# Kernel tuning notes

Measured on AMD Instinct MI355X. Metric: run time of the kernel, lower is better.

Reference implementation:

```python
import jax, jax.numpy as jnp
import numpy as np

EMBED_DIM = 1024
NUM_HEADS = 16
HEAD_DIM = EMBED_DIM // NUM_HEADS


def setup_inputs() -> dict:
    key = jax.random.key(0)
    k1, k2, k3, k4, k5 = jax.random.split(key, 5)
    C = EMBED_DIM
    x = jax.random.normal(k1, (4, 2048, C), dtype=jnp.float32)
    s = 1.0 / np.sqrt(C)
    qkv_w = jax.random.uniform(k2, (3 * C, C), jnp.float32, -s, s)
    qkv_b = jax.random.uniform(k3, (3 * C,), jnp.float32, -s, s)
    proj_w = jax.random.uniform(k4, (C, C), jnp.float32, -s, s)
    proj_b = jax.random.uniform(k5, (C,), jnp.float32, -s, s)
    return {"x": x, "qkv_w": qkv_w, "qkv_b": qkv_b, "proj_w": proj_w, "proj_b": proj_b}


def reference(x, qkv_w, qkv_b, proj_w, proj_b):
    B, T, C = x.shape
    H, D = NUM_HEADS, HEAD_DIM
    qkv = jnp.einsum('btc,oc->bto', x, qkv_w) + qkv_b  # [B,T,3C]
    q, k, v = jnp.split(qkv, 3, axis=2)
    # [B,T,C] -> [B,H,T,D]
    q = q.reshape(B, T, H, D).transpose(0, 2, 1, 3)
    k = k.reshape(B, T, H, D).transpose(0, 2, 1, 3)
    v = v.reshape(B, T, H, D).transpose(0, 2, 1, 3)
    scores = jnp.einsum('bhqd,bhkd->bhqk', q, k) / jnp.sqrt(jnp.float32(D)).astype(q.dtype)
    causal = jnp.tril(jnp.ones((T, T), dtype=bool))
    scores = jnp.where(causal[None, None], scores, jnp.finfo(scores.dtype).min)
    attn = jax.nn.softmax(scores, axis=-1)
    out = jnp.einsum('bhqk,bhkd->bhqd', attn, v)
    out = out.transpose(0, 2, 1, 3).reshape(B, T, C)
    return jnp.einsum('btc,oc->bto', out, proj_w) + proj_b
```

## Files before the change

kernel.cpp:

```cpp
#include <hip/hip_runtime.h>

#define EMBED 1024
#define C3    3072
#define NHEAD 16
#define HDIM  64
#define BB    4
#define TT    2048
#define MTOK  8192

typedef __bf16 bf16;
typedef __bf16 bf16x4 __attribute__((ext_vector_type(4)));
typedef __bf16 bf16x8 __attribute__((ext_vector_type(8)));
typedef float  f32x4  __attribute__((ext_vector_type(4)));
typedef float  f32x16 __attribute__((ext_vector_type(16)));
typedef unsigned int u32;

__device__ __forceinline__ void gload_lds16(const bf16* g, bf16* l) {
  __builtin_amdgcn_global_load_lds((__attribute__((address_space(1))) void*)g,
                                   (__attribute__((address_space(3))) void*)l,
                                   16, 0, 0);
}

__device__ __forceinline__ u32 pkbf(float lo, float hi_) {
  union { bf16 h[2]; u32 w; } u;
  u.h[0] = (bf16)lo; u.h[1] = (bf16)hi_;
  return u.w;
}

__global__ __launch_bounds__(256) void cvt_kernel(const float* __restrict__ in,
                                                  bf16* __restrict__ out, int n) {
  int i = (blockIdx.x * blockDim.x + threadIdx.x) * 4;
  if (i >= n) return;
  float4 v = *reinterpret_cast<const float4*>(in + i);
  bf16x4 o;
  o[0] = (bf16)v.x; o[1] = (bf16)v.y; o[2] = (bf16)v.z; o[3] = (bf16)v.w;
  *reinterpret_cast<bf16x4*>(out + i) = o;
}

__global__ __launch_bounds__(256) void gemm_qkv(const bf16* __restrict__ A,
                                                const bf16* __restrict__ W,
                                                const float* __restrict__ bias,
                                                bf16* __restrict__ Qh,
                                                bf16* __restrict__ Kh,
                                                bf16* __restrict__ VhT) {
  const int K = EMBED;
  __shared__ __align__(16) bf16 lA[128 * 32];
  __shared__ __align__(16) bf16 lB[128 * 32];
  const int tid  = threadIdx.x;
  const int lane = tid & 63;
  const int wave = tid >> 6;
  const int wm   = (wave >> 1) * 64;
  const int wn   = (wave & 1) * 64;
  const int bn0  = blockIdx.x * 128;
  const int bm0  = blockIdx.y * 128;
  const int l15  = lane & 15, lg = lane >> 4;
  const int srow = tid >> 2;
  const int sseg = tid & 3;

  f32x4 acc[4][4] = {};

  for (int kt = 0; kt < K; kt += 32) {
#pragma unroll
    for (int c = 0; c < 2; ++c) {
      int row = c * 64 + srow;
      gload_lds16(A + (size_t)(bm0 + row) * K + kt + sseg * 8, &lA[(c * 256 + tid) * 8]);
      gload_lds16(W + (size_t)(bn0 + row) * K + kt + sseg * 8, &lB[(c * 256 + tid) * 8]);
    }
    __syncthreads();
    bf16x8 af[4], bf_[4];
#pragma unroll
    for (int i = 0; i < 4; ++i)
      af[i] = *reinterpret_cast<const bf16x8*>(&lA[(wm + i * 16 + l15) * 32 + lg * 8]);
#pragma unroll
    for (int j = 0; j < 4; ++j)
      bf_[j] = *reinterpret_cast<const bf16x8*>(&lB[(wn + j * 16 + l15) * 32 + lg * 8]);
#pragma unroll
    for (int i = 0; i < 4; ++i)
#pragma unroll
      for (int j = 0; j < 4; ++j)
        acc[i][j] = __builtin_amdgcn_mfma_f32_16x16x32_bf16(af[i], bf_[j], acc[i][j], 0, 0, 0);
    __syncthreads();
  }

  const int sec = bn0 >> 10;
#pragma unroll
  for (int i = 0; i < 4; ++i)
#pragma unroll
    for (int j = 0; j < 4; ++j) {
      const int col = bn0 + wn + j * 16 + l15;
      const float bs = bias[col];
      const int c2 = col & 1023, hh = c2 >> 6, dd = c2 & 63;
      const int rowb = bm0 + wm + i * 16 + lg * 4;
      const int bb = rowb >> 11, t0 = rowb & 2047;
      const int bh = bb * 16 + hh;
      if (sec < 2) {
        bf16* dst = (sec ? Kh : Qh) + ((size_t)bh * TT + t0) * HDIM + dd;
#pragma unroll
        for (int r = 0; r < 4; ++r) dst[(size_t)r * HDIM] = (bf16)(acc[i][j][r] + bs);
      } else {
        bf16x4 o4;
#pragma unroll
        for (int r = 0; r < 4; ++r) o4[r] = (bf16)(acc[i][j][r] + bs);
        *reinterpret_cast<bf16x4*>(VhT + ((size_t)bh * HDIM + dd) * TT + t0) = o4;
      }
    }
}

__global__ __launch_bounds__(256) void gemm_bt(const bf16* __restrict__ A,
                                               const bf16* __restrict__ W,
                                               const float* __restrict__ bias,
                                               float* __restrict__ Cf,
                                               int M, int N, int K) {
  __shared__ __align__(16) bf16 lA[128 * 32];
  __shared__ __align__(16) bf16 lB[128 * 32];
  const int tid  = threadIdx.x;
  const int lane = tid & 63;
  const int wave = tid >> 6;
  const int wm   = (wave >> 1) * 64;
  const int wn   = (wave & 1) * 64;
  const int bn0  = blockIdx.x * 128;
  const int bm0  = blockIdx.y * 128;
  const int l15  = lane & 15, lg = lane >> 4;
  const int srow = tid >> 2;
  const int sseg = tid & 3;

  f32x4 acc[4][4] = {};

  for (int kt = 0; kt < K; kt += 32) {
#pragma unroll
    for (int c = 0; c < 2; ++c) {
      int row = c * 64 + srow;
      gload_lds16(A + (size_t)(bm0 + row) * K + kt + sseg * 8, &lA[(c * 256 + tid) * 8]);
      gload_lds16(W + (size_t)(bn0 + row) * K + kt + sseg * 8, &lB[(c * 256 + tid) * 8]);
    }
    __syncthreads();
    bf16x8 af[4], bf_[4];
#pragma unroll
    for (int i = 0; i < 4; ++i)
      af[i] = *reinterpret_cast<const bf16x8*>(&lA[(wm + i * 16 + l15) * 32 + lg * 8]);
#pragma unroll
    for (int j = 0; j < 4; ++j)
      bf_[j] = *reinterpret_cast<const bf16x8*>(&lB[(wn + j * 16 + l15) * 32 + lg * 8]);
#pragma unroll
    for (int i = 0; i < 4; ++i)
#pragma unroll
      for (int j = 0; j < 4; ++j)
        acc[i][j] = __builtin_amdgcn_mfma_f32_16x16x32_bf16(af[i], bf_[j], acc[i][j], 0, 0, 0);
    __syncthreads();
  }

#pragma unroll
  for (int i = 0; i < 4; ++i)
#pragma unroll
    for (int j = 0; j < 4; ++j) {
      int col = bn0 + wn + j * 16 + l15;
      float bs = bias[col];
#pragma unroll
      for (int r = 0; r < 4; ++r) {
        int row = bm0 + wm + i * 16 + lg * 4 + r;
        Cf[(size_t)row * N + col] = acc[i][j][r] + bs;
      }
    }
}

__device__ __forceinline__ void attn_tile(const char* kbase, const char* vbase,
                                          const bf16x8 (&qfr)[4], f32x16 (&oacc)[2],
                                          float& mrun, float& srun,
                                          const int kv0, const int q0w,
                                          const int l31, const int hi, const int swz) {
  f32x16 s0 = {}, s1 = {};
  __builtin_amdgcn_s_setprio(1);
#pragma unroll
  for (int dc = 0; dc < 4; ++dc) {
    bf16x8 kf = *reinterpret_cast<const bf16x8*>(
        kbase + l31 * 128 + (((2 * dc + hi) * 16) ^ swz));
    s0 = __builtin_amdgcn_mfma_f32_32x32x16_bf16(kf, qfr[dc], s0, 0, 0, 0);
  }
#pragma unroll
  for (int dc = 0; dc < 4; ++dc) {
    bf16x8 kf = *reinterpret_cast<const bf16x8*>(
        kbase + (32 + l31) * 128 + (((2 * dc + hi) * 16) ^ swz));
    s1 = __builtin_amdgcn_mfma_f32_32x32x16_bf16(kf, qfr[dc], s1, 0, 0, 0);
  }
  __builtin_amdgcn_s_setprio(0);

  if (kv0 + 63 > q0w) {
    const int qg = q0w + l31;
#pragma unroll
    for (int r = 0; r < 16; ++r) {
      const int kvb = kv0 + (r & 3) + 8 * (r >> 2) + 4 * hi;
      if (kvb > qg)      s0[r] = -3e38f;
      if (kvb + 32 > qg) s1[r] = -3e38f;
    }
  }

  float m8[8];
#pragma unroll
  for (int i = 0; i < 8; ++i)
    m8[i] = fmaxf(fmaxf(s0[i], s0[i + 8]), fmaxf(s1[i], s1[i + 8]));
#pragma unroll
  for (int st = 4; st > 0; st >>= 1)
#pragma unroll
    for (int i = 0; i < st; ++i) m8[i] = fmaxf(m8[i], m8[i + st]);
  float mx = fmaxf(m8[0], __shfl_xor(m8[0], 32));

  float mref = mrun;
  if (!__all(mx <= mrun + 8.0f)) {
    const float mnew = fmaxf(mrun, mx);
    const float corr = __builtin_amdgcn_exp2f(mrun - mnew);
    mrun = mnew; mref = mnew;
    srun *= corr;
#pragma unroll
    for (int r = 0; r < 16; ++r) { oacc[0][r] *= corr; oacc[1][r] *= corr; }
  }

  float psum = 0.0f;
#pragma unroll
  for (int r = 0; r < 16; ++r) {
    s0[r] = __builtin_amdgcn_exp2f(s0[r] - mref);
    s1[r] = __builtin_amdgcn_exp2f(s1[r] - mref);
    psum += s0[r] + s1[r];
  }
  srun += psum;

  union { u32 w[4]; bf16x8 v; } pw[4];
#pragma unroll
  for (int cl = 0; cl < 2; ++cl) {
    {
      u32 a01 = pkbf(s0[8 * cl + 0], s0[8 * cl + 1]);
      u32 a23 = pkbf(s0[8 * cl + 2], s0[8 * cl + 3]);
      u32 b01 = pkbf(s0[8 * cl + 4], s0[8 * cl + 5]);
      u32 b23 = pkbf(s0[8 * cl + 6], s0[8 * cl + 7]);
      asm("v_permlane32_swap_b32 %0, %1" : "+v"(a01), "+v"(b01));
      asm("v_permlane32_swap_b32 %0, %1" : "+v"(a23), "+v"(b23));
      pw[cl].w[0] = a01; pw[cl].w[1] = a23; pw[cl].w[2] = b01; pw[cl].w[3] = b23;
    }
    {
      u32 a01 = pkbf(s1[8 * cl + 0], s1[8 * cl + 1]);
      u32 a23 = pkbf(s1[8 * cl + 2], s1[8 * cl + 3]);
      u32 b01 = pkbf(s1[8 * cl + 4], s1[8 * cl + 5]);
      u32 b23 = pkbf(s1[8 * cl + 6], s1[8 * cl + 7]);
      asm("v_permlane32_swap_b32 %0, %1" : "+v"(a01), "+v"(b01));
      asm("v_permlane32_swap_b32 %0, %1" : "+v"(a23), "+v"(b23));
      pw[2 + cl].w[0] = a01; pw[2 + cl].w[1] = a23; pw[2 + cl].w[2] = b01; pw[2 + cl].w[3] = b23;
    }
  }

  __builtin_amdgcn_s_setprio(1);
#pragma unroll
  for (int dh = 0; dh < 2; ++dh) {
    const char* vrow = vbase + (32 * dh + l31) * 128;
#pragma unroll
    for (int c = 0; c < 4; ++c) {
      bf16x8 vf = *reinterpret_cast<const bf16x8*>(vrow + (((2 * c + hi) * 16) ^ swz));
      oacc[dh] = __builtin_amdgcn_mfma_f32_32x32x16_bf16(vf, pw[c].v, oacc[dh], 0, 0, 0);
    }
  }
  __builtin_amdgcn_s_setprio(0);
}

__global__ __launch_bounds__(256, 2) void attn_kernel(const bf16* __restrict__ Qh,
                                                      const bf16* __restrict__ Kh,
                                                      const bf16* __restrict__ VhT,
                                                      bf16* __restrict__ aout) {
  __shared__ __align__(16) bf16 lK[2][64 * 64];
  __shared__ __align__(16) bf16 lVT[2][64 * 64];
  const int tid  = threadIdx.x;
  const int lane = tid & 63, wave = tid >> 6;
  const int l31  = lane & 31;
  const int hi   = lane >> 5;
  const int bid  = blockIdx.x;
  const int bh   = bid & 63;
  const int p    = bid >> 6;
  const int qtH  = 15 - p, qtL = p;
  const int b    = bh >> 4, h = bh & 15;
  const int q0H  = qtH * 128 + wave * 32;
  const int q0L  = qtL * 128 + wave * 32;
  const size_t tb = (size_t)b * TT;
  const int swz  = (l31 & 7) << 4;

  const float QSCALE = 0.18033688011112042f;
  bf16x8 qfrH[4], qfrL[4];
  {
    const bf16* qrowH = Qh + ((size_t)bh * TT + q0H + l31) * HDIM;
    const bf16* qrowL = Qh + ((size_t)bh * TT + q0L + l31) * HDIM;
#pragma unroll
    for (int dc = 0; dc < 4; ++dc) {
      bf16x8 vH = *reinterpret_cast<const bf16x8*>(qrowH + dc * 16 + hi * 8);
      bf16x8 vL = *reinterpret_cast<const bf16x8*>(qrowL + dc * 16 + hi * 8);
      bf16x8 oH, oL;
#pragma unroll
      for (int j = 0; j < 8; ++j) {
        oH[j] = (bf16)((float)vH[j] * QSCALE);
        oL[j] = (bf16)((float)vL[j] * QSCALE);
      }
      qfrH[dc] = oH; qfrL[dc] = oL;
    }
  }

  f32x16 oaccH[2] = {}, oaccL[2] = {};
  float mH = -3e38f, sH = 0.0f, mL = -3e38f, sL = 0.0f;

  const int r0 = tid >> 3, sg = tid & 7;
  const bf16* kS0 = Kh + ((size_t)bh * TT + r0) * HDIM + (size_t)(sg ^ (r0 & 7)) * 8;
  const bf16* kS1 = Kh + ((size_t)bh * TT + 32 + r0) * HDIM + (size_t)(sg ^ (r0 & 7)) * 8;
  const bf16* vS0 = VhT + ((size_t)bh * HDIM + r0) * TT + (size_t)(sg ^ (r0 & 7)) * 8;
  const bf16* vS1 = VhT + ((size_t)bh * HDIM + 32 + r0) * TT + (size_t)(sg ^ (r0 & 7)) * 8;

  const int nkv = 2 * qtH + 2;

  gload_lds16(kS0, &lK[0][tid * 8]);
  gload_lds16(kS1, &lK[0][(tid + 256) * 8]);
  gload_lds16(vS0, &lVT[0][tid * 8]);
  gload_lds16(vS1, &lVT[0][(tid + 256) * 8]);
  __syncthreads();

  int cur = 0;
  for (int t = 0; t < nkv; ++t) {
    const int kv0 = t * 64;
    if (t + 1 < nkv) {
      const int kvn = kv0 + 64;
      gload_lds16(kS0 + (size_t)kvn * HDIM, &lK[cur ^ 1][tid * 8]);
      gload_lds16(kS1 + (size_t)kvn * HDIM, &lK[cur ^ 1][(tid + 256) * 8]);
      gload_lds16(vS0 + kvn, &lVT[cur ^ 1][tid * 8]);
      gload_lds16(vS1 + kvn, &lVT[cur ^ 1][(tid + 256) * 8]);
    }

    const char* kbase = (const char*)&lK[cur][0];
    const char* vbase = (const char*)&lVT[cur][0];
    if (kv0 <= q0H + 31)
      attn_tile(kbase, vbase, qfrH, oaccH, mH, sH, kv0, q0H, l31, hi, swz);
    if (kv0 <= q0L + 31)
      attn_tile(kbase, vbase, qfrL, oaccL, mL, sL, kv0, q0L, l31, hi, swz);

    __syncthreads();
    cur ^= 1;
  }

#pragma unroll
  for (int band = 0; band < 2; ++band) {
    const f32x16* oacc = band ? oaccL : oaccH;
    float sr = band ? sL : sH;
    sr += __shfl_xor(sr, 32);
    const float inv = 1.0f / sr;
    const int q = (band ? q0L : q0H) + l31;
    bf16* orow = aout + (tb + q) * (size_t)EMBED + h * HDIM;
#pragma unroll
    for (int dh = 0; dh < 2; ++dh)
#pragma unroll
      for (int rb = 0; rb < 4; ++rb) {
        bf16x4 o4;
#pragma unroll
        for (int k = 0; k < 4; ++k) o4[k] = (bf16)(oacc[dh][4 * rb + k] * inv);
        *reinterpret_cast<bf16x4*>(orow + 32 * dh + 8 * rb + 4 * hi) = o4;
      }
  }
}

extern "C" void kernel_launch(void* const* d_in, const int* in_sizes, int n_in,
                              void* d_out, int out_size, void* d_ws, size_t ws_size,
                              hipStream_t stream) {
  const float* x      = (const float*)d_in[0];
  const float* qkv_w  = (const float*)d_in[1];
  const float* qkv_b  = (const float*)d_in[2];
  const float* proj_w = (const float*)d_in[3];
  const float* proj_b = (const float*)d_in[4];
  float* out = (float*)d_out;

  const size_t QSZ = (size_t)BB * NHEAD * TT * HDIM;
  char* ws = (char*)d_ws;
  bf16* xb    = (bf16*)ws;
  bf16* wqkv  = xb + (size_t)MTOK * EMBED;
  bf16* wproj = wqkv + (size_t)C3 * EMBED;
  bf16* Qh    = wproj + (size_t)EMBED * EMBED;
  bf16* Kh    = Qh + QSZ;
  bf16* VhT   = Kh + QSZ;
  bf16* aob   = xb;

  cvt_kernel<<<dim3((MTOK * EMBED / 4 + 255) / 256), dim3(256), 0, stream>>>(x, xb, MTOK * EMBED);
  cvt_kernel<<<dim3((C3 * EMBED / 4 + 255) / 256), dim3(256), 0, stream>>>(qkv_w, wqkv, C3 * EMBED);
  cvt_kernel<<<dim3((EMBED * EMBED / 4 + 255) / 256), dim3(256), 0, stream>>>(proj_w, wproj, EMBED * EMBED);

  gemm_qkv<<<dim3(C3 / 128, MTOK / 128), dim3(256), 0, stream>>>(xb, wqkv, qkv_b, Qh, Kh, VhT);

  attn_kernel<<<dim3(512), dim3(256), 0, stream>>>(Qh, Kh, VhT, aob);

  gemm_bt<<<dim3(EMBED / 128, MTOK / 128), dim3(256), 0, stream>>>(
      aob, wproj, proj_b, out, MTOK, EMBED, EMBED);
}
```

Measured before the change: 177.4 us.

## Drop LDS staging in attention, per-wave KV loop; widen GEMM K-tile with swizzle

```diff
diff --git a/kernel.cpp b/kernel.cpp
--- a/kernel.cpp
+++ b/kernel.cpp
@@ -26,6 +26,8 @@
   u.h[0] = (bf16)lo; u.h[1] = (bf16)hi_;
   return u.w;
 }
+
+union upw { u32 w[4]; bf16x8 v; };
 
 __global__ __launch_bounds__(256) void cvt_kernel(const float* __restrict__ in,
                                                   bf16* __restrict__ out, int n) {
@@ -37,50 +39,70 @@
   *reinterpret_cast<bf16x4*>(out + i) = o;
 }
 
+__device__ __forceinline__ void gemm_core(const bf16* __restrict__ A,
+                                          const bf16* __restrict__ W,
+                                          int K, int bm0, int bn0,
+                                          int wm, int wn, int l15, int lg,
+                                          f32x4 (&acc)[4][4]) {
+  __shared__ __align__(16) bf16 lA[128 * 64];
+  __shared__ __align__(16) bf16 lB[128 * 64];
+  const int tid  = threadIdx.x;
+  const int grow = tid >> 3;
+  const int gseg = tid & 7;
+
+  for (int kt = 0; kt < K; kt += 64) {
+#pragma unroll
+    for (int r = 0; r < 4; ++r) {
+      const int row = r * 32 + grow;
+      const int seg = gseg ^ (row & 7);
+      gload_lds16(A + (size_t)(bm0 + row) * K + kt + seg * 8, &lA[(r * 256 + tid) * 8]);
+      gload_lds16(W + (size_t)(bn0 + row) * K + kt + seg * 8, &lB[(r * 256 + tid) * 8]);
+    }
+    __syncthreads();
+    const char* Ab = (const char*)lA;
+    const char* Bb = (const char*)lB;
+#pragma unroll
+    for (int kk = 0; kk < 2; ++kk) {
+      bf16x8 af[4], bf_[4];
+#pragma unroll
+      for (int i = 0; i < 4; ++i) {
+        const int row = wm + i * 16 + l15;
+        af[i] = *reinterpret_cast<const bf16x8*>(
+            Ab + row * 128 + ((kk * 64 + lg * 16) ^ ((row & 7) << 4)));
+      }
+#pragma unroll
+      for (int j = 0; j < 4; ++j) {
+        const int row = wn + j * 16 + l15;
+        bf_[j] = *reinterpret_cast<const bf16x8*>(
+            Bb + row * 128 + ((kk * 64 + lg * 16) ^ ((row & 7) << 4)));
+      }
+#pragma unroll
+      for (int i = 0; i < 4; ++i)
+#pragma unroll
+        for (int j = 0; j < 4; ++j)
+          acc[i][j] = __builtin_amdgcn_mfma_f32_16x16x32_bf16(af[i], bf_[j],
+                                                              acc[i][j], 0, 0, 0);
+    }
+    __syncthreads();
+  }
+}
+
 __global__ __launch_bounds__(256) void gemm_qkv(const bf16* __restrict__ A,
                                                 const bf16* __restrict__ W,
                                                 const float* __restrict__ bias,
                                                 bf16* __restrict__ Qh,
                                                 bf16* __restrict__ Kh,
                                                 bf16* __restrict__ VhT) {
-  const int K = EMBED;
-  __shared__ __align__(16) bf16 lA[128 * 32];
-  __shared__ __align__(16) bf16 lB[128 * 32];
   const int tid  = threadIdx.x;
-  const int lane = tid & 63;
-  const int wave = tid >> 6;
+  const int lane = tid & 63, wave = tid >> 6;
   const int wm   = (wave >> 1) * 64;
   const int wn   = (wave & 1) * 64;
   const int bn0  = blockIdx.x * 128;
   const int bm0  = blockIdx.y * 128;
   const int l15  = lane & 15, lg = lane >> 4;
-  const int srow = tid >> 2;
-  const int sseg = tid & 3;
 
   f32x4 acc[4][4] = {};
-
-  for (int kt = 0; kt < K; kt += 32) {
-#pragma unroll
-    for (int c = 0; c < 2; ++c) {
-      int row = c * 64 + srow;
-      gload_lds16(A + (size_t)(bm0 + row) * K + kt + sseg * 8, &lA[(c * 256 + tid) * 8]);
-      gload_lds16(W + (size_t)(bn0 + row) * K + kt + sseg * 8, &lB[(c * 256 + tid) * 8]);
-    }
-    __syncthreads();
-    bf16x8 af[4], bf_[4];
-#pragma unroll
-    for (int i = 0; i < 4; ++i)
-      af[i] = *reinterpret_cast<const bf16x8*>(&lA[(wm + i * 16 + l15) * 32 + lg * 8]);
-#pragma unroll
-    for (int j = 0; j < 4; ++j)
-      bf_[j] = *reinterpret_cast<const bf16x8*>(&lB[(wn + j * 16 + l15) * 32 + lg * 8]);
-#pragma unroll
-    for (int i = 0; i < 4; ++i)
-#pragma unroll
-      for (int j = 0; j < 4; ++j)
-        acc[i][j] = __builtin_amdgcn_mfma_f32_16x16x32_bf16(af[i], bf_[j], acc[i][j], 0, 0, 0);
-    __syncthreads();
-  }
+  gemm_core(A, W, EMBED, bm0, bn0, wm, wn, l15, lg, acc);
 
   const int sec = bn0 >> 10;
 #pragma unroll
@@ -111,43 +133,16 @@
                                                const float* __restrict__ bias,
                                                float* __restrict__ Cf,
                                                int M, int N, int K) {
-  __shared__ __align__(16) bf16 lA[128 * 32];
-  __shared__ __align__(16) bf16 lB[128 * 32];
   const int tid  = threadIdx.x;
-  const int lane = tid & 63;
-  const int wave = tid >> 6;
+  const int lane = tid & 63, wave = tid >> 6;
   const int wm   = (wave >> 1) * 64;
   const int wn   = (wave & 1) * 64;
   const int bn0  = blockIdx.x * 128;
   const int bm0  = blockIdx.y * 128;
   const int l15  = lane & 15, lg = lane >> 4;
-  const int srow = tid >> 2;
-  const int sseg = tid & 3;
 
   f32x4 acc[4][4] = {};
-
-  for (int kt = 0; kt < K; kt += 32) {
-#pragma unroll
-    for (int c = 0; c < 2; ++c) {
-      int row = c * 64 + srow;
-      gload_lds16(A + (size_t)(bm0 + row) * K + kt + sseg * 8, &lA[(c * 256 + tid) * 8]);
-      gload_lds16(W + (size_t)(bn0 + row) * K + kt + sseg * 8, &lB[(c * 256 + tid) * 8]);
-    }
-    __syncthreads();
-    bf16x8 af[4], bf_[4];
-#pragma unroll
-    for (int i = 0; i < 4; ++i)
-      af[i] = *reinterpret_cast<const bf16x8*>(&lA[(wm + i * 16 + l15) * 32 + lg * 8]);
-#pragma unroll
-    for (int j = 0; j < 4; ++j)
-      bf_[j] = *reinterpret_cast<const bf16x8*>(&lB[(wn + j * 16 + l15) * 32 + lg * 8]);
-#pragma unroll
-    for (int i = 0; i < 4; ++i)
-#pragma unroll
-      for (int j = 0; j < 4; ++j)
-        acc[i][j] = __builtin_amdgcn_mfma_f32_16x16x32_bf16(af[i], bf_[j], acc[i][j], 0, 0, 0);
-    __syncthreads();
-  }
+  gemm_core(A, W, K, bm0, bn0, wm, wn, l15, lg, acc);
 
 #pragma unroll
   for (int i = 0; i < 4; ++i)
@@ -163,47 +158,26 @@
     }
 }
 
-__device__ __forceinline__ void attn_tile(const char* kbase, const char* vbase,
-                                          const bf16x8 (&qfr)[4], f32x16 (&oacc)[2],
-                                          float& mrun, float& srun,
-                                          const int kv0, const int q0w,
-                                          const int l31, const int hi, const int swz) {
-  f32x16 s0 = {}, s1 = {};
-  __builtin_amdgcn_s_setprio(1);
-#pragma unroll
-  for (int dc = 0; dc < 4; ++dc) {
-    bf16x8 kf = *reinterpret_cast<const bf16x8*>(
-        kbase + l31 * 128 + (((2 * dc + hi) * 16) ^ swz));
-    s0 = __builtin_amdgcn_mfma_f32_32x32x16_bf16(kf, qfr[dc], s0, 0, 0, 0);
-  }
-#pragma unroll
-  for (int dc = 0; dc < 4; ++dc) {
-    bf16x8 kf = *reinterpret_cast<const bf16x8*>(
-        kbase + (32 + l31) * 128 + (((2 * dc + hi) * 16) ^ swz));
-    s1 = __builtin_amdgcn_mfma_f32_32x32x16_bf16(kf, qfr[dc], s1, 0, 0, 0);
-  }
-  __builtin_amdgcn_s_setprio(0);
-
-  if (kv0 + 63 > q0w) {
+__device__ __forceinline__ void sm_pack(f32x16& s, float& mrun, float& srun,
+                                        f32x16 (&oacc)[2], upw (&pw)[2],
+                                        const int kv0, const int q0w,
+                                        const int l31, const int hi) {
+  if (kv0 + 31 > q0w) {
     const int qg = q0w + l31;
 #pragma unroll
     for (int r = 0; r < 16; ++r) {
       const int kvb = kv0 + (r & 3) + 8 * (r >> 2) + 4 * hi;
-      if (kvb > qg)      s0[r] = -3e38f;
-      if (kvb + 32 > qg) s1[r] = -3e38f;
-    }
-  }
-
+      if (kvb > qg) s[r] = -3e38f;
+    }
+  }
   float m8[8];
 #pragma unroll
-  for (int i = 0; i < 8; ++i)
-    m8[i] = fmaxf(fmaxf(s0[i], s0[i + 8]), fmaxf(s1[i], s1[i + 8]));
+  for (int i = 0; i < 8; ++i) m8[i] = fmaxf(s[i], s[i + 8]);
 #pragma unroll
   for (int st = 4; st > 0; st >>= 1)
 #pragma unroll
     for (int i = 0; i < st; ++i) m8[i] = fmaxf(m8[i], m8[i + st]);
-  float mx = fmaxf(m8[0], __shfl_xor(m8[0], 32));
-
+  const float mx = fmaxf(m8[0], __shfl_xor(m8[0], 32));
   float mref = mrun;
   if (!__all(mx <= mrun + 8.0f)) {
     const float mnew = fmaxf(mrun, mx);
@@ -213,58 +187,29 @@
 #pragma unroll
     for (int r = 0; r < 16; ++r) { oacc[0][r] *= corr; oacc[1][r] *= corr; }
   }
-
   float psum = 0.0f;
 #pragma unroll
   for (int r = 0; r < 16; ++r) {
-    s0[r] = __builtin_amdgcn_exp2f(s0[r] - mref);
-    s1[r] = __builtin_amdgcn_exp2f(s1[r] - mref);
-    psum += s0[r] + s1[r];
+    s[r] = __builtin_amdgcn_exp2f(s[r] - mref);
+    psum += s[r];
   }
   srun += psum;
-
-  union { u32 w[4]; bf16x8 v; } pw[4];
 #pragma unroll
   for (int cl = 0; cl < 2; ++cl) {
-    {
-      u32 a01 = pkbf(s0[8 * cl + 0], s0[8 * cl + 1]);
-      u32 a23 = pkbf(s0[8 * cl + 2], s0[8 * cl + 3]);
-      u32 b01 = pkbf(s0[8 * cl + 4], s0[8 * cl + 5]);
-      u32 b23 = pkbf(s0[8 * cl + 6], s0[8 * cl + 7]);
-      asm("v_permlane32_swap_b32 %0, %1" : "+v"(a01), "+v"(b01));
-      asm("v_permlane32_swap_b32 %0, %1" : "+v"(a23), "+v"(b23));
-      pw[cl].w[0] = a01; pw[cl].w[1] = a23; pw[cl].w[2] = b01; pw[cl].w[3] = b23;
-    }
-    {
-      u32 a01 = pkbf(s1[8 * cl + 0], s1[8 * cl + 1]);
-      u32 a23 = pkbf(s1[8 * cl + 2], s1[8 * cl + 3]);
-      u32 b01 = pkbf(s1[8 * cl + 4], s1[8 * cl + 5]);
-      u32 b23 = pkbf(s1[8 * cl + 6], s1[8 * cl + 7]);
-      asm("v_permlane32_swap_b32 %0, %1" : "+v"(a01), "+v"(b01));
-      asm("v_permlane32_swap_b32 %0, %1" : "+v"(a23), "+v"(b23));
-      pw[2 + cl].w[0] = a01; pw[2 + cl].w[1] = a23; pw[2 + cl].w[2] = b01; pw[2 + cl].w[3] = b23;
-    }
-  }
-
-  __builtin_amdgcn_s_setprio(1);
-#pragma unroll
-  for (int dh = 0; dh < 2; ++dh) {
-    const char* vrow = vbase + (32 * dh + l31) * 128;
-#pragma unroll
-    for (int c = 0; c < 4; ++c) {
-      bf16x8 vf = *reinterpret_cast<const bf16x8*>(vrow + (((2 * c + hi) * 16) ^ swz));
-      oacc[dh] = __builtin_amdgcn_mfma_f32_32x32x16_bf16(vf, pw[c].v, oacc[dh], 0, 0, 0);
-    }
-  }
-  __builtin_amdgcn_s_setprio(0);
+    u32 a01 = pkbf(s[8 * cl + 0], s[8 * cl + 1]);
+    u32 a23 = pkbf(s[8 * cl + 2], s[8 * cl + 3]);
+    u32 b01 = pkbf(s[8 * cl + 4], s[8 * cl + 5]);
+    u32 b23 = pkbf(s[8 * cl + 6], s[8 * cl + 7]);
+    asm("v_permlane32_swap_b32 %0, %1" : "+v"(a01), "+v"(b01));
+    asm("v_permlane32_swap_b32 %0, %1" : "+v"(a23), "+v"(b23));
+    pw[cl].w[0] = a01; pw[cl].w[1] = a23; pw[cl].w[2] = b01; pw[cl].w[3] = b23;
+  }
 }
 
 __global__ __launch_bounds__(256, 2) void attn_kernel(const bf16* __restrict__ Qh,
                                                       const bf16* __restrict__ Kh,
                                                       const bf16* __restrict__ VhT,
                                                       bf16* __restrict__ aout) {
-  __shared__ __align__(16) bf16 lK[2][64 * 64];
-  __shared__ __align__(16) bf16 lVT[2][64 * 64];
   const int tid  = threadIdx.x;
   const int lane = tid & 63, wave = tid >> 6;
   const int l31  = lane & 31;
@@ -277,7 +222,9 @@
   const int q0H  = qtH * 128 + wave * 32;
   const int q0L  = qtL * 128 + wave * 32;
   const size_t tb = (size_t)b * TT;
-  const int swz  = (l31 & 7) << 4;
+
+  const bf16* Kbh = Kh + (size_t)bh * TT * HDIM;
+  const bf16* Vbh = VhT + (size_t)bh * HDIM * TT;
 
   const float QSCALE = 0.18033688011112042f;
   bf16x8 qfrH[4], qfrL[4];
@@ -299,48 +246,70 @@
   }
 
   f32x16 oaccH[2] = {}, oaccL[2] = {};
-  float mH = -3e38f, sH = 0.0f, mL = -3e38f, sL = 0.0f;
-
-  const int r0 = tid >> 3, sg = tid & 7;
-  const bf16* kS0 = Kh + ((size_t)bh * TT + r0) * HDIM + (size_t)(sg ^ (r0 & 7)) * 8;
-  const bf16* kS1 = Kh + ((size_t)bh * TT + 32 + r0) * HDIM + (size_t)(sg ^ (r0 & 7)) * 8;
-  const bf16* vS0 = VhT + ((size_t)bh * HDIM + r0) * TT + (size_t)(sg ^ (r0 & 7)) * 8;
-  const bf16* vS1 = VhT + ((size_t)bh * HDIM + 32 + r0) * TT + (size_t)(sg ^ (r0 & 7)) * 8;
-
-  const int nkv = 2 * qtH + 2;
-
-  gload_lds16(kS0, &lK[0][tid * 8]);
-  gload_lds16(kS1, &lK[0][(tid + 256) * 8]);
-  gload_lds16(vS0, &lVT[0][tid * 8]);
-  gload_lds16(vS1, &lVT[0][(tid + 256) * 8]);
-  __syncthreads();
-
-  int cur = 0;
-  for (int t = 0; t < nkv; ++t) {
-    const int kv0 = t * 64;
-    if (t + 1 < nkv) {
-      const int kvn = kv0 + 64;
-      gload_lds16(kS0 + (size_t)kvn * HDIM, &lK[cur ^ 1][tid * 8]);
-      gload_lds16(kS1 + (size_t)kvn * HDIM, &lK[cur ^ 1][(tid + 256) * 8]);
-      gload_lds16(vS0 + kvn, &lVT[cur ^ 1][tid * 8]);
-      gload_lds16(vS1 + kvn, &lVT[cur ^ 1][(tid + 256) * 8]);
-    }
-
-    const char* kbase = (const char*)&lK[cur][0];
-    const char* vbase = (const char*)&lVT[cur][0];
-    if (kv0 <= q0H + 31)
-      attn_tile(kbase, vbase, qfrH, oaccH, mH, sH, kv0, q0H, l31, hi, swz);
-    if (kv0 <= q0L + 31)
-      attn_tile(kbase, vbase, qfrL, oaccL, mL, sL, kv0, q0L, l31, hi, swz);
-
-    __syncthreads();
-    cur ^= 1;
+  float mH = -3e38f, sHr = 0.0f, mL = -3e38f, sLr = 0.0f;
+
+  const int nkvH = (q0H >> 5) + 1;
+  const int nkvL = (q0L >> 5) + 1;
+
+  for (int t = 0; t < nkvH; ++t) {
+    const int kv0 = t * 32;
+    const bool doL = (t < nkvL);
+
+    bf16x8 kf[4];
+#pragma unroll
+    for (int dc = 0; dc < 4; ++dc)
+      kf[dc] = *reinterpret_cast<const bf16x8*>(
+          Kbh + (size_t)(kv0 + l31) * HDIM + dc * 16 + hi * 8);
+    bf16x8 vf[2][2];
+#pragma unroll
+    for (int dh = 0; dh < 2; ++dh)
+#pragma unroll
+      for (int c = 0; c < 2; ++c)
+        vf[dh][c] = *reinterpret_cast<const bf16x8*>(
+            Vbh + (size_t)(32 * dh + l31) * TT + kv0 + c * 16 + hi * 8);
+
+    f32x16 sH = {};
+    __builtin_amdgcn_s_setprio(1);
+#pragma unroll
+    for (int dc = 0; dc < 4; ++dc)
+      sH = __builtin_amdgcn_mfma_f32_32x32x16_bf16(kf[dc], qfrH[dc], sH, 0, 0, 0);
+    __builtin_amdgcn_s_setprio(0);
+    upw pwH[2];
+    sm_pack(sH, mH, sHr, oaccH, pwH, kv0, q0H, l31, hi);
+
+    upw pwL[2];
+    if (doL) {
+      f32x16 sL = {};
+      __builtin_amdgcn_s_setprio(1);
+#pragma unroll
+      for (int dc = 0; dc < 4; ++dc)
+        sL = __builtin_amdgcn_mfma_f32_32x32x16_bf16(kf[dc], qfrL[dc], sL, 0, 0, 0);
+      __builtin_amdgcn_s_setprio(0);
+      sm_pack(sL, mL, sLr, oaccL, pwL, kv0, q0L, l31, hi);
+    }
+
+    __builtin_amdgcn_s_setprio(1);
+#pragma unroll
+    for (int dh = 0; dh < 2; ++dh)
+#pragma unroll
+      for (int c = 0; c < 2; ++c)
+        oaccH[dh] = __builtin_amdgcn_mfma_f32_32x32x16_bf16(vf[dh][c], pwH[c].v,
+                                                            oaccH[dh], 0, 0, 0);
+    if (doL) {
+#pragma unroll
+      for (int dh = 0; dh < 2; ++dh)
+#pragma unroll
+        for (int c = 0; c < 2; ++c)
+          oaccL[dh] = __builtin_amdgcn_mfma_f32_32x32x16_bf16(vf[dh][c], pwL[c].v,
+                                                              oaccL[dh], 0, 0, 0);
+    }
+    __builtin_amdgcn_s_setprio(0);
   }
 
 #pragma unroll
   for (int band = 0; band < 2; ++band) {
     const f32x16* oacc = band ? oaccL : oaccH;
-    float sr = band ? sL : sH;
+    float sr = band ? sLr : sHr;
     sr += __shfl_xor(sr, 32);
     const float inv = 1.0f / sr;
     const int q = (band ? q0L : q0H) + l31;
```

Result: slower. 215.9 us (+21.7%).
